# Kernel tuning notes

Hardware: AMD Instinct MI355X
Metric: run time of the kernel (lower is better)

## Reference

```python
import jax, jax.numpy as jnp
import numpy as np

B, T, I, H, E = 256, 128, 512, 1024, 256


def setup_inputs() -> dict:
    key = jax.random.key(0)
    ks = jax.random.split(key, 14)
    s = lambda *d: 1.0 / np.sqrt(d[-1])
    inp = {
        "x": jax.random.normal(ks[0], (B, T, I), jnp.float32),
        # encoder LSTMCell(I, H): weights [4H, *], gate order i,f,g,o (torch)
        "enc_Wih": jax.random.uniform(ks[1], (4 * H, I), jnp.float32, -s(H), s(H)),
        "enc_Whh": jax.random.uniform(ks[2], (4 * H, H), jnp.float32, -s(H), s(H)),
        "enc_bih": jax.random.uniform(ks[3], (4 * H,), jnp.float32, -s(H), s(H)),
        "enc_bhh": jax.random.uniform(ks[4], (4 * H,), jnp.float32, -s(H), s(H)),
        # enc_fc: H -> E
        "encfc_W": jax.random.uniform(ks[5], (E, H), jnp.float32, -s(H), s(H)),
        "encfc_b": jax.random.uniform(ks[6], (E,), jnp.float32, -s(H), s(H)),
        # dec_fc: E -> H
        "decfc_W": jax.random.uniform(ks[7], (H, E), jnp.float32, -s(E), s(E)),
        "decfc_b": jax.random.uniform(ks[8], (H,), jnp.float32, -s(E), s(E)),
        # decoder LSTMCell(H + I, I)
        "dec_Wih": jax.random.uniform(ks[9], (4 * I, H + I), jnp.float32, -s(I), s(I)),
        "dec_Whh": jax.random.uniform(ks[10], (4 * I, I), jnp.float32, -s(I), s(I)),
        "dec_bih": jax.random.uniform(ks[11], (4 * I,), jnp.float32, -s(I), s(I)),
        "dec_bhh": jax.random.uniform(ks[12], (4 * I,), jnp.float32, -s(I), s(I)),
    }
    return inp


def _gates(pre):
    i, f, g, o = jnp.split(pre, 4, axis=-1)
    return jax.nn.sigmoid(i), jax.nn.sigmoid(f), jnp.tanh(g), jax.nn.sigmoid(o)


def reference(x, enc_Wih, enc_Whh, enc_bih, enc_bhh, encfc_W, encfc_b,
              decfc_W, decfc_b, dec_Wih, dec_Whh, dec_bih, dec_bhh):
    b = x.shape[0]
    # ---- encoder: precompute input projections for all timesteps ----
    x_proj = jnp.einsum('btd,gd->tbg', x, enc_Wih) + (enc_bih + enc_bhh)  # [T,B,4H]

    def enc_step(carry, xp):
        h, c = carry
        i, f, g, o = _gates(xp + h @ enc_Whh.T)
        c = f * c + i * g
        h = o * jnp.tanh(c)
        return (h, c), None

    h0 = jnp.zeros((b, H), x.dtype)
    c0 = jnp.zeros((b, H), x.dtype)
    (_, c_final), _ = jax.lax.scan(enc_step, (h0, c0), x_proj)

    # NB: original code names the returned (h, c) as (o_t_enc, h_t_enc), so
    # embd is computed from the final CELL state -- replicated faithfully.
    embd = jax.nn.relu(c_final @ encfc_W.T + encfc_b)                # [B,E]
    dec_first_hidden = jax.nn.relu(embd @ decfc_W.T + decfc_b)       # [B,H]

    # ---- decoder: input at each step is cat(dec_first_hidden, h_prev) ----
    # (eval path: teacher forcing disabled; dec states init to zeros)
    fixed = dec_first_hidden @ dec_Wih[:, :H].T + (dec_bih + dec_bhh)  # [B,4I]
    W_rec = dec_Wih[:, H:] + dec_Whh  # input second-half and hidden are both h_prev

    def dec_step(carry, _):
        h, c = carry
        i, f, g, o = _gates(fixed + h @ W_rec.T)
        c = f * c + i * g
        h = o * jnp.tanh(c)
        return (h, c), h

    hd0 = jnp.zeros((b, I), x.dtype)
    cd0 = jnp.zeros((b, I), x.dtype)
    _, hs = jax.lax.scan(dec_step, (hd0, cd0), None, length=x.shape[1])  # [T,B,I]
    outputs = jnp.transpose(hs[::-1], (1, 0, 2))  # reversed, [B,T,I]
    return outputs, embd
```

## Files before the change

### kernel.cpp

```cpp
#include <hip/hip_runtime.h>
#include <hip/hip_fp16.h>


#define B_ 256
#define T_ 128
#define I_ 512
#define H_ 1024
#define E_ 256

#define ENC_STEP 262144
#define DEC_STEP 131072
#define SENT32 0x7C7C7C7Cu

typedef _Float16 half8 __attribute__((ext_vector_type(8)));
typedef float floatx4 __attribute__((ext_vector_type(4)));

__device__ __forceinline__ float sigmoidf_(float x) { return 1.0f / (1.0f + __expf(-x)); }
__device__ __forceinline__ float tanhf_(float x) {
    x = fminf(fmaxf(x, -15.0f), 15.0f);
    float e = __expf(2.0f * x);
    return (e - 1.0f) / (e + 1.0f);
}

union HU { unsigned long long u[2]; half8 h; };

__device__ __forceinline__ void ld_chunk(const _Float16* p, HU& v) {
    const unsigned long long* q = (const unsigned long long*)p;
    v.u[0] = __hip_atomic_load(q,     __ATOMIC_RELAXED, __HIP_MEMORY_SCOPE_AGENT);
    v.u[1] = __hip_atomic_load(q + 1, __ATOMIC_RELAXED, __HIP_MEMORY_SCOPE_AGENT);
}
__device__ __forceinline__ int chunk_ok(const HU& v) {
    unsigned a = (unsigned)v.u[0], b = (unsigned)(v.u[0] >> 32);
    unsigned c = (unsigned)v.u[1], d = (unsigned)(v.u[1] >> 32);
    return (int)((a != SENT32) & (b != SENT32) & (c != SENT32) & (d != SENT32));
}
template <int STRIDE>
__device__ __forceinline__ void load_grp(const _Float16* base, HU v[4]) {
#pragma unroll
    for (int m = 0; m < 4; ++m) ld_chunk(base + (size_t)m * STRIDE, v[m]);
}
template <int STRIDE>
__device__ __forceinline__ void fix_grp(const _Float16* base, HU v[4]) {
    while (!(chunk_ok(v[0]) & chunk_ok(v[1]) & chunk_ok(v[2]) & chunk_ok(v[3]))) {
        __builtin_amdgcn_s_sleep(1);
        load_grp<STRIDE>(base, v);
    }
}

__device__ __forceinline__ half8 ldg_h8_sc1(const _Float16* p) {
    HU v; ld_chunk(p, v); return v.h;
}
__device__ __forceinline__ void stg_h2_sc1(_Float16* p, float a, float b) {
    union { _Float16 h[2]; unsigned int u; } v;
    v.h[0] = (_Float16)a; v.h[1] = (_Float16)b;
    __hip_atomic_store((unsigned int*)p, v.u, __ATOMIC_RELAXED, __HIP_MEMORY_SCOPE_AGENT);
}
__device__ __forceinline__ void wait_vm0() {
    asm volatile("s_waitcnt vmcnt(0)" ::: "memory");
}
__device__ __forceinline__ void poll_rg(int* flags, int rgbase, int lane, int target) {
    while (__hip_atomic_load(&flags[rgbase + lane], __ATOMIC_RELAXED, __HIP_MEMORY_SCOPE_AGENT) < target)
        __builtin_amdgcn_s_sleep(1);
    asm volatile("" ::: "memory");
}

__global__ void shuffle_x_kernel(const float* __restrict__ x, _Float16* __restrict__ xf) {
    const int gg   = blockIdx.x * 256 + threadIdx.x;
    const int tile = gg >> 6;
    const int lane = gg & 63;
    const int t  = tile >> 8;
    const int rt = (tile >> 4) & 15;
    const int kc = tile & 15;
    const int b  = rt * 16 + (lane & 15);
    const int j0 = kc * 32 + ((lane >> 4) << 3);
    const float* src = x + ((size_t)b * T_ + t) * I_ + j0;
    float4 f0 = *(const float4*)src;
    float4 f1 = *(const float4*)(src + 4);
    half8 h = { (_Float16)f0.x, (_Float16)f0.y, (_Float16)f0.z, (_Float16)f0.w,
                (_Float16)f1.x, (_Float16)f1.y, (_Float16)f1.z, (_Float16)f1.w };
    *(half8*)(xf + (size_t)tile * 512 + lane * 8) = h;
}

__global__ __launch_bounds__(256) void small_gemm_kernel(
    const float* __restrict__ A, int lda,
    const float* __restrict__ W, int ldw,
    const float* __restrict__ b1, const float* __restrict__ b2,
    float* __restrict__ out, int N, int K, int relu)
{
    __shared__ float sA2[32][33];
    __shared__ float sW2[32][33];
    int tid = threadIdx.x;
    int tx = tid & 15, ty = tid >> 4;
    int m0 = blockIdx.y * 32, n0 = blockIdx.x * 32;
    float acc[2][2] = {};
    for (int k0 = 0; k0 < K; k0 += 32) {
        __syncthreads();
#pragma unroll
        for (int i = 0; i < 4; ++i) {
            int e = tid + i * 256;
            int r = e >> 5, c = e & 31;
            sA2[r][c] = A[(size_t)(m0 + r) * lda + k0 + c];
            sW2[r][c] = W[(size_t)(n0 + r) * ldw + k0 + c];
        }
        __syncthreads();
#pragma unroll
        for (int k = 0; k < 32; ++k) {
            float a0 = sA2[ty * 2][k], a1 = sA2[ty * 2 + 1][k];
            float w0 = sW2[tx * 2][k], w1 = sW2[tx * 2 + 1][k];
            acc[0][0] += a0 * w0; acc[0][1] += a0 * w1;
            acc[1][0] += a1 * w0; acc[1][1] += a1 * w1;
        }
    }
#pragma unroll
    for (int i = 0; i < 2; ++i)
#pragma unroll
        for (int j = 0; j < 2; ++j) {
            int m = m0 + ty * 2 + i, n = n0 + tx * 2 + j;
            float v = acc[i][j] + b1[n] + (b2 ? b2[n] : 0.0f);
            if (relu) v = fmaxf(v, 0.0f);
            out[(size_t)m * N + n] = v;
        }
}

__global__ __launch_bounds__(256, 1) void enc_persist(
    const _Float16* __restrict__ xf,
    const float* __restrict__ Wih, const float* __restrict__ Whh,
    const float* __restrict__ bih, const float* __restrict__ bhh,
    _Float16* __restrict__ hbuf, float* __restrict__ c_out, int* __restrict__ flags)
{
    const int tid  = threadIdx.x;
    const int wave = tid >> 6, lane = tid & 63;
    const int q = lane >> 4, n15 = lane & 15;
    const int blk = blockIdx.x;
    const int rg = blk >> 6, cc = blk & 63;

    half8 bw[4][12];
#pragma unroll
    for (int g = 0; g < 4; ++g) {
        const int jc = g * H_ + cc * 16 + n15;
#pragma unroll
        for (int kc = 0; kc < 12; ++kc) {
            const int k = (4 * kc + wave) * 32 + q * 8;
            const float* src = (k < I_) ? (Wih + (size_t)jc * I_ + k)
                                        : (Whh + (size_t)jc * H_ + (k - I_));
            float4 f0 = *(const float4*)src;
            float4 f1 = *(const float4*)(src + 4);
            bw[g][kc] = half8{(_Float16)f0.x, (_Float16)f0.y, (_Float16)f0.z, (_Float16)f0.w,
                              (_Float16)f1.x, (_Float16)f1.y, (_Float16)f1.z, (_Float16)f1.w};
        }
    }

    const int hcp = tid & 7;
    const int rT  = tid >> 3;
    float breg[4][2];
#pragma unroll
    for (int g = 0; g < 4; ++g)
#pragma unroll
        for (int e = 0; e < 2; ++e) {
            const int j = g * H_ + cc * 16 + 2 * hcp + e;
            breg[g][e] = bih[j] + bhh[j];
        }
    float creg[2][2] = {{0.f, 0.f}, {0.f, 0.f}};

    __shared__ float preT[4][64][35];
    const size_t laneoff = (size_t)lane * 8;

    for (int s = 0; s < T_; ++s) {
        const _Float16* __restrict__ hcur = hbuf + (size_t)(s & 1) * 262144;
        _Float16* __restrict__ hnxt = hbuf + (size_t)((s + 1) & 1) * 262144;

        floatx4 acc[4][4];
#pragma unroll
        for (int m = 0; m < 4; ++m)
#pragma unroll
            for (int n = 0; n < 4; ++n) acc[m][n] = floatx4{0.f, 0.f, 0.f, 0.f};

        half8 X[4][4];
#pragma unroll
        for (int kc = 0; kc < 4; ++kc)
#pragma unroll
            for (int m = 0; m < 4; ++m)
                X[kc][m] = *(const half8*)(xf + (((size_t)s * 16 + rg * 4 + m) * 16
                                                + (4 * kc + wave)) * 512 + laneoff);
#pragma unroll
        for (int kc = 0; kc < 2; ++kc)
#pragma unroll
            for (int n = 0; n < 4; ++n)
#pragma unroll
                for (int m = 0; m < 4; ++m)
                    acc[m][n] = __builtin_amdgcn_mfma_f32_16x16x32_f16(
                        X[kc][m], bw[n][kc], acc[m][n], 0, 0, 0);

        poll_rg(flags, rg * 64, lane, 4 * s);

        half8 Hb[4][4];
#pragma unroll
        for (int kc = 4; kc < 8; ++kc)
#pragma unroll
            for (int m = 0; m < 4; ++m)
                Hb[kc - 4][m] = ldg_h8_sc1(hcur + ((size_t)(rg * 4 + m) * 32
                                                   + (4 * kc + wave - 16)) * 512 + laneoff);

#pragma unroll
        for (int kc = 2; kc < 4; ++kc)
#pragma unroll
            for (int n = 0; n < 4; ++n)
#pragma unroll
                for (int m = 0; m < 4; ++m)
                    acc[m][n] = __builtin_amdgcn_mfma_f32_16x16x32_f16(
                        X[kc][m], bw[n][kc], acc[m][n], 0, 0, 0);

#pragma unroll
        for (int kc = 4; kc < 12; ++kc) {
            const int sl = kc & 3;
#pragma unroll
            for (int n = 0; n < 4; ++n)
#pragma unroll
                for (int m = 0; m < 4; ++m)
                    acc[m][n] = __builtin_amdgcn_mfma_f32_16x16x32_f16(
                        Hb[sl][m], bw[n][kc], acc[m][n], 0, 0, 0);
            if (kc < 8) {
#pragma unroll
                for (int m = 0; m < 4; ++m)
                    Hb[sl][m] = ldg_h8_sc1(hcur + ((size_t)(rg * 4 + m) * 32
                                                   + (4 * (kc + 4) + wave - 16)) * 512 + laneoff);
            }
        }

#pragma unroll
        for (int p = 0; p < 2; ++p) {
            if (p) __syncthreads();
#pragma unroll
            for (int m = 0; m < 2; ++m)
#pragma unroll
                for (int n = 0; n < 4; ++n)
#pragma unroll
                    for (int r = 0; r < 4; ++r)
                        preT[wave][n * 16 + n15][m * 16 + q * 4 + r] = acc[p * 2 + m][n][r];
            __syncthreads();
            float pg[4][2];
#pragma unroll
            for (int g = 0; g < 4; ++g)
#pragma unroll
                for (int e = 0; e < 2; ++e) {
                    const int col = g * 16 + 2 * hcp + e;
                    pg[g][e] = preT[0][col][rT] + preT[1][col][rT]
                             + preT[2][col][rT] + preT[3][col][rT] + breg[g][e];
                }
            float hv[2];
#pragma unroll
            for (int e = 0; e < 2; ++e) {
                const float ig = sigmoidf_(pg[0][e]);
                const float fg = sigmoidf_(pg[1][e]);
                const float gg = tanhf_(pg[2][e]);
                const float og = sigmoidf_(pg[3][e]);
                const float c  = fg * creg[p][e] + ig * gg;
                creg[p][e] = c;
                hv[e] = og * tanhf_(c);
            }
            const int row = p * 32 + rT;
            const int j   = cc * 16 + 2 * hcp;
            const int kch = j >> 5, j5 = j & 31;
            const int lt  = (row & 15) | ((j5 >> 3) << 4);
            stg_h2_sc1(hnxt + ((size_t)(rg * 4 + (row >> 4)) * 32 + kch) * 512
                            + lt * 8 + (j5 & 7), hv[0], hv[1]);
        }

        wait_vm0();
        if (lane == 0)
            __hip_atomic_fetch_add(&flags[blk], 1, __ATOMIC_RELAXED, __HIP_MEMORY_SCOPE_AGENT);
        __syncthreads();
    }

#pragma unroll
    for (int p = 0; p < 2; ++p)
        *(float2*)(c_out + (size_t)(rg * 64 + p * 32 + rT) * H_ + cc * 16 + 2 * hcp)
            = float2{creg[p][0], creg[p][1]};
}

__global__ __launch_bounds__(256, 1) void dec_df(
    const float* __restrict__ dWih, const float* __restrict__ dWhh,
    const float* __restrict__ fixedb,
    _Float16* __restrict__ hbuf, float* __restrict__ out)
{
    const int tid  = threadIdx.x;
    const int wave = tid >> 6, lane = tid & 63;
    const int q = lane >> 4, n15 = lane & 15;
    const int blk = blockIdx.x;
    const int rg = blk >> 6, cc = blk & 63;

    half8 bw[2][4];
#pragma unroll
    for (int n = 0; n < 2; ++n) {
        const int jc = (n * 2 + (n15 >> 3)) * I_ + cc * 8 + (n15 & 7);
#pragma unroll
        for (int kc = 0; kc < 4; ++kc) {
            const int k = wave * 128 + kc * 32 + q * 8;
            const float* s0 = dWih + (size_t)jc * (H_ + I_) + H_ + k;
            const float* s1 = dWhh + (size_t)jc * I_ + k;
            float4 a0 = *(const float4*)s0, a1 = *(const float4*)(s0 + 4);
            float4 b0 = *(const float4*)s1, b1 = *(const float4*)(s1 + 4);
            bw[n][kc] = half8{(_Float16)(a0.x + b0.x), (_Float16)(a0.y + b0.y),
                              (_Float16)(a0.z + b0.z), (_Float16)(a0.w + b0.w),
                              (_Float16)(a1.x + b1.x), (_Float16)(a1.y + b1.y),
                              (_Float16)(a1.z + b1.z), (_Float16)(a1.w + b1.w)};
        }
    }

    const int hcp = tid & 3;
    const int rT  = tid >> 2;
    const int brow = rg * 64 + rT;
    float fx[4][2];
#pragma unroll
    for (int g = 0; g < 4; ++g)
#pragma unroll
        for (int e = 0; e < 2; ++e)
            fx[g][e] = fixedb[(size_t)brow * (4 * I_) + g * I_ + cc * 8 + 2 * hcp + e];
    float creg2[2] = {0.f, 0.f};

    __shared__ float preT[4][32][67];
    const size_t laneoff = (size_t)lane * 8;

    for (int s = 0; s < T_; ++s) {
        const _Float16* __restrict__ hcur = hbuf + (size_t)s * DEC_STEP;
        _Float16* __restrict__ hnxt = hbuf + (size_t)(s + 1) * DEC_STEP;

        HU Hb[4][4];
#pragma unroll
        for (int kc = 0; kc < 4; ++kc)
            load_grp<16 * 512>(hcur + ((size_t)(rg * 4) * 16 + (wave * 4 + kc)) * 512
                                    + laneoff, Hb[kc]);

        floatx4 acc[4][2];
#pragma unroll
        for (int m = 0; m < 4; ++m)
#pragma unroll
            for (int n = 0; n < 2; ++n) acc[m][n] = floatx4{0.f, 0.f, 0.f, 0.f};
#pragma unroll
        for (int kc = 0; kc < 4; ++kc) {
            fix_grp<16 * 512>(hcur + ((size_t)(rg * 4) * 16 + (wave * 4 + kc)) * 512
                                   + laneoff, Hb[kc]);
#pragma unroll
            for (int n = 0; n < 2; ++n)
#pragma unroll
                for (int m = 0; m < 4; ++m)
                    acc[m][n] = __builtin_amdgcn_mfma_f32_16x16x32_f16(
                        Hb[kc][m].h, bw[n][kc], acc[m][n], 0, 0, 0);
        }

#pragma unroll
        for (int p = 0; p < 2; ++p) {
            if (p) __syncthreads();
#pragma unroll
            for (int m = 0; m < 2; ++m)
#pragma unroll
                for (int n = 0; n < 2; ++n)
#pragma unroll
                    for (int r = 0; r < 4; ++r)
                        preT[wave][n * 16 + n15][m * 16 + q * 4 + r] = acc[p * 2 + m][n][r];
            __syncthreads();
            if ((rT >> 5) == p) {
                const int rl = rT & 31;
                float pg[4][2];
#pragma unroll
                for (int g = 0; g < 4; ++g)
#pragma unroll
                    for (int e = 0; e < 2; ++e) {
                        const int col = (g >> 1) * 16 + (g & 1) * 8 + 2 * hcp + e;
                        pg[g][e] = preT[0][col][rl] + preT[1][col][rl]
                                 + preT[2][col][rl] + preT[3][col][rl] + fx[g][e];
                    }
                float hv[2];
#pragma unroll
                for (int e = 0; e < 2; ++e) {
                    const float ig = sigmoidf_(pg[0][e]);
                    const float fg = sigmoidf_(pg[1][e]);
                    const float gg = tanhf_(pg[2][e]);
                    const float og = sigmoidf_(pg[3][e]);
                    const float c  = fg * creg2[e] + ig * gg;
                    creg2[e] = c;
                    hv[e] = og * tanhf_(c);
                }
                *(float2*)(out + ((size_t)brow * T_ + (T_ - 1 - s)) * I_ + cc * 8 + 2 * hcp)
                    = float2{hv[0], hv[1]};
                const int j = cc * 8 + 2 * hcp;
                const int kch = j >> 5, j5 = j & 31;
                const int lt  = (rT & 15) | ((j5 >> 3) << 4);
                stg_h2_sc1(hnxt + ((size_t)(rg * 4 + (rT >> 4)) * 16 + kch) * 512
                                + lt * 8 + (j5 & 7), hv[0], hv[1]);
            }
        }
        __syncthreads();
    }
}

__global__ __launch_bounds__(256, 1) void dec_persist(
    const float* __restrict__ dWih, const float* __restrict__ dWhh,
    const float* __restrict__ fixedb,
    _Float16* __restrict__ hbuf, float* __restrict__ out, int* __restrict__ flags)
{
    const int tid  = threadIdx.x;
    const int wave = tid >> 6, lane = tid & 63;
    const int q = lane >> 4, n15 = lane & 15;
    const int blk = blockIdx.x;
    const int rg = blk >> 6, cc = blk & 63;

    half8 bw[2][4];
#pragma unroll
    for (int n = 0; n < 2; ++n) {
        const int jc = (n * 2 + (n15 >> 3)) * I_ + cc * 8 + (n15 & 7);
#pragma unroll
        for (int kc = 0; kc < 4; ++kc) {
            const int k = wave * 128 + kc * 32 + q * 8;
            const float* s0 = dWih + (size_t)jc * (H_ + I_) + H_ + k;
            const float* s1 = dWhh + (size_t)jc * I_ + k;
            float4 a0 = *(const float4*)s0, a1 = *(const float4*)(s0 + 4);
            float4 b0 = *(const float4*)s1, b1 = *(const float4*)(s1 + 4);
            bw[n][kc] = half8{(_Float16)(a0.x + b0.x), (_Float16)(a0.y + b0.y),
                              (_Float16)(a0.z + b0.z), (_Float16)(a0.w + b0.w),
                              (_Float16)(a1.x + b1.x), (_Float16)(a1.y + b1.y),
                              (_Float16)(a1.z + b1.z), (_Float16)(a1.w + b1.w)};
        }
    }

    const int hcp = tid & 3;
    const int rT  = tid >> 2;
    const int brow = rg * 64 + rT;
    float fx[4][2];
#pragma unroll
    for (int g = 0; g < 4; ++g)
#pragma unroll
        for (int e = 0; e < 2; ++e)
            fx[g][e] = fixedb[(size_t)brow * (4 * I_) + g * I_ + cc * 8 + 2 * hcp + e];
    float creg2[2] = {0.f, 0.f};

    __shared__ float preT[4][32][67];
    const size_t laneoff = (size_t)lane * 8;

    for (int s = 0; s < T_; ++s) {
        const _Float16* __restrict__ hcur = hbuf + (size_t)(s & 1) * 131072;
        _Float16* __restrict__ hnxt = hbuf + (size_t)((s + 1) & 1) * 131072;

        poll_rg(flags, rg * 64, lane, s);

        half8 Hb[4][4];
#pragma unroll
        for (int kc = 0; kc < 4; ++kc)
#pragma unroll
            for (int m = 0; m < 4; ++m)
                Hb[kc][m] = ldg_h8_sc1(hcur + ((size_t)(rg * 4 + m) * 16
                                               + (wave * 4 + kc)) * 512 + laneoff);
        floatx4 acc[4][2];
#pragma unroll
        for (int m = 0; m < 4; ++m)
#pragma unroll
            for (int n = 0; n < 2; ++n) acc[m][n] = floatx4{0.f, 0.f, 0.f, 0.f};
#pragma unroll
        for (int kc = 0; kc < 4; ++kc)
#pragma unroll
            for (int n = 0; n < 2; ++n)
#pragma unroll
                for (int m = 0; m < 4; ++m)
                    acc[m][n] = __builtin_amdgcn_mfma_f32_16x16x32_f16(
                        Hb[kc][m], bw[n][kc], acc[m][n], 0, 0, 0);

#pragma unroll
        for (int p = 0; p < 2; ++p) {
            if (p) __syncthreads();
#pragma unroll
            for (int m = 0; m < 2; ++m)
#pragma unroll
                for (int n = 0; n < 2; ++n)
#pragma unroll
                    for (int r = 0; r < 4; ++r)
                        preT[wave][n * 16 + n15][m * 16 + q * 4 + r] = acc[p * 2 + m][n][r];
            __syncthreads();
            if ((rT >> 5) == p) {
                const int rl = rT & 31;
                float pg[4][2];
#pragma unroll
                for (int g = 0; g < 4; ++g)
#pragma unroll
                    for (int e = 0; e < 2; ++e) {
                        const int col = (g >> 1) * 16 + (g & 1) * 8 + 2 * hcp + e;
                        pg[g][e] = preT[0][col][rl] + preT[1][col][rl]
                                 + preT[2][col][rl] + preT[3][col][rl] + fx[g][e];
                    }
                float hv[2];
#pragma unroll
                for (int e = 0; e < 2; ++e) {
                    const float ig = sigmoidf_(pg[0][e]);
                    const float fg = sigmoidf_(pg[1][e]);
                    const float gg = tanhf_(pg[2][e]);
                    const float og = sigmoidf_(pg[3][e]);
                    const float c  = fg * creg2[e] + ig * gg;
                    creg2[e] = c;
                    hv[e] = og * tanhf_(c);
                }
                *(float2*)(out + ((size_t)brow * T_ + (T_ - 1 - s)) * I_ + cc * 8 + 2 * hcp)
                    = float2{hv[0], hv[1]};
                const int j = cc * 8 + 2 * hcp;
                const int kch = j >> 5, j5 = j & 31;
                const int lt  = (rT & 15) | ((j5 >> 3) << 4);
                stg_h2_sc1(hnxt + ((size_t)(rg * 4 + (rT >> 4)) * 16 + kch) * 512
                                + lt * 8 + (j5 & 7), hv[0], hv[1]);
            }
        }

        wait_vm0();
        __syncthreads();
        if (tid == 0)
            __hip_atomic_store(&flags[blk], s + 1, __ATOMIC_RELAXED, __HIP_MEMORY_SCOPE_AGENT);
    }
}

extern "C" void kernel_launch(void* const* d_in, const int* in_sizes, int n_in,
                              void* d_out_v, int out_size, void* d_ws, size_t ws_size,
                              hipStream_t stream) {
    (void)in_sizes; (void)n_in; (void)out_size;
    const float* x    = (const float*)d_in[0];
    const float* eWih = (const float*)d_in[1];
    const float* eWhh = (const float*)d_in[2];
    const float* ebih = (const float*)d_in[3];
    const float* ebhh = (const float*)d_in[4];
    const float* efcW = (const float*)d_in[5];
    const float* efcb = (const float*)d_in[6];
    const float* dfcW = (const float*)d_in[7];
    const float* dfcb = (const float*)d_in[8];
    const float* dWih = (const float*)d_in[9];
    const float* dWhh = (const float*)d_in[10];
    const float* dbih = (const float*)d_in[11];
    const float* dbhh = (const float*)d_in[12];
    float* d_out = (float*)d_out_v;

    char* ws = (char*)d_ws;
    size_t off = 0;
    auto carve = [&](size_t bytes) {
        char* p = ws + off;
        off += (bytes + 255) & ~(size_t)255;
        return p;
    };

    const size_t xf_b  = (size_t)B_ * T_ * I_ * 2;
    const size_t hbE_b = (size_t)2 * ENC_STEP * 2;
    const size_t hbD_b = (size_t)(T_ + 1) * DEC_STEP * 2;
    const size_t ce_b  = (size_t)B_ * H_ * 4;
    const size_t fxb_b = (size_t)B_ * 4 * I_ * 4;
    const size_t d1_b  = (size_t)B_ * H_ * 4;
    const size_t need_primary = xf_b + hbE_b + hbD_b + ce_b + fxb_b + d1_b + 8192;

    float* embd = d_out + (size_t)B_ * T_ * I_;

    if (ws_size == 0 || ws_size >= need_primary) {
        _Float16* xf     = (_Float16*)carve(xf_b);
        _Float16* hbufE  = (_Float16*)carve(hbE_b);
        _Float16* hbufD  = (_Float16*)carve(hbD_b);
        float*    c_e    = (float*)carve(ce_b);
        float*    fixedb = (float*)carve(fxb_b);
        float*    dec1   = (float*)carve(d1_b);
        int*      flagsE = (int*)carve(256 * 4);

        hipMemsetAsync(flagsE, 0, 256 * 4, stream);
        hipMemsetAsync(hbufE, 0, (size_t)ENC_STEP * 2, stream);
        hipMemsetAsync(hbufD, 0, (size_t)DEC_STEP * 2, stream);
        hipMemsetAsync((char*)hbufD + (size_t)DEC_STEP * 2, 0x7C, (size_t)T_ * DEC_STEP * 2, stream);

        shuffle_x_kernel<<<dim3(8192), 256, 0, stream>>>(x, xf);
        enc_persist<<<dim3(256), 256, 0, stream>>>(xf, eWih, eWhh, ebih, ebhh,
                                                   hbufE, c_e, flagsE);
        small_gemm_kernel<<<dim3(E_ / 32, B_ / 32), 256, 0, stream>>>(
            c_e, H_, efcW, H_, efcb, nullptr, embd, E_, H_, 1);
        small_gemm_kernel<<<dim3(H_ / 32, B_ / 32), 256, 0, stream>>>(
            embd, E_, dfcW, E_, dfcb, nullptr, dec1, H_, E_, 1);
        small_gemm_kernel<<<dim3(4 * I_ / 32, B_ / 32), 256, 0, stream>>>(
            dec1, H_, dWih, H_ + I_, dbih, dbhh, fixedb, 4 * I_, H_, 0);
        dec_df<<<dim3(256), 256, 0, stream>>>(dWih, dWhh, fixedb, hbufD, d_out);
    } else {
        _Float16* xf     = (_Float16*)carve(xf_b);
        _Float16* hbufE  = (_Float16*)carve((size_t)2 * ENC_STEP * 2);
        _Float16* hbufD  = (_Float16*)carve((size_t)2 * DEC_STEP * 2);
        float*    c_e    = (float*)carve(ce_b);
        float*    fixedb = (float*)carve(fxb_b);
        float*    dec1   = (float*)carve(d1_b);
        int*      flagsE = (int*)carve(256 * 4);
        int*      flagsD = (int*)carve(256 * 4);

        hipMemsetAsync(flagsE, 0, 256 * 4, stream);
        hipMemsetAsync(flagsD, 0, 256 * 4, stream);
        hipMemsetAsync(hbufE, 0, (size_t)ENC_STEP * 2, stream);
        hipMemsetAsync(hbufD, 0, (size_t)DEC_STEP * 2, stream);

        shuffle_x_kernel<<<dim3(8192), 256, 0, stream>>>(x, xf);
        enc_persist<<<dim3(256), 256, 0, stream>>>(xf, eWih, eWhh, ebih, ebhh,
                                                   hbufE, c_e, flagsE);
        small_gemm_kernel<<<dim3(E_ / 32, B_ / 32), 256, 0, stream>>>(
            c_e, H_, efcW, H_, efcb, nullptr, embd, E_, H_, 1);
        small_gemm_kernel<<<dim3(H_ / 32, B_ / 32), 256, 0, stream>>>(
            embd, E_, dfcW, E_, dfcb, nullptr, dec1, H_, E_, 1);
        small_gemm_kernel<<<dim3(4 * I_ / 32, B_ / 32), 256, 0, stream>>>(
            dec1, H_, dWih, H_ + I_, dbih, dbhh, fixedb, 4 * I_, H_, 0);
        dec_persist<<<dim3(256), 256, 0, stream>>>(dWih, dWhh, fixedb,
                                                   hbufD, d_out, flagsD);
    }
}
```

Before: 1.653 ms.

## Re-tile persistent encoder to 512-thread blocks with 32 rows by 32 hidden columns

The encoder persistent kernel now runs 8 waves per block, and each block owns a 32-row by 32-hidden-column tile instead of 64 rows by 16 columns. Each wave holds fewer K-slices of the weights and does less serial MFMA work per step. The new h values are staged in shared memory so they go out as coalesced 32-bit stores, and each block now waits on only 32 producer flags. The cost is a larger cross-wave reduction over 8 partial sums in LDS, and the fallback path keeps the old kernel under a new name.

```diff
diff --git a/kernel.cpp b/kernel.cpp
--- a/kernel.cpp
+++ b/kernel.cpp
@@ -22,7 +22,7 @@
     return (e - 1.0f) / (e + 1.0f);
 }
 
-union HU { unsigned long long u[2]; half8 h; };
+union HU { unsigned long long u[2]; unsigned v[4]; half8 h; };
 
 __device__ __forceinline__ void ld_chunk(const _Float16* p, HU& v) {
     const unsigned long long* q = (const unsigned long long*)p;
@@ -30,9 +30,8 @@
     v.u[1] = __hip_atomic_load(q + 1, __ATOMIC_RELAXED, __HIP_MEMORY_SCOPE_AGENT);
 }
 __device__ __forceinline__ int chunk_ok(const HU& v) {
-    unsigned a = (unsigned)v.u[0], b = (unsigned)(v.u[0] >> 32);
-    unsigned c = (unsigned)v.u[1], d = (unsigned)(v.u[1] >> 32);
-    return (int)((a != SENT32) & (b != SENT32) & (c != SENT32) & (d != SENT32));
+    return (int)((v.v[0] != SENT32) & (v.v[1] != SENT32)
+               & (v.v[2] != SENT32) & (v.v[3] != SENT32));
 }
 template <int STRIDE>
 __device__ __forceinline__ void load_grp(const _Float16* base, HU v[4]) {
@@ -54,6 +53,9 @@
     union { _Float16 h[2]; unsigned int u; } v;
     v.h[0] = (_Float16)a; v.h[1] = (_Float16)b;
     __hip_atomic_store((unsigned int*)p, v.u, __ATOMIC_RELAXED, __HIP_MEMORY_SCOPE_AGENT);
+}
+__device__ __forceinline__ void stg_u32_sc1(_Float16* p, unsigned v) {
+    __hip_atomic_store((unsigned int*)p, v, __ATOMIC_RELAXED, __HIP_MEMORY_SCOPE_AGENT);
 }
 __device__ __forceinline__ void wait_vm0() {
     asm volatile("s_waitcnt vmcnt(0)" ::: "memory");
@@ -122,7 +124,7 @@
         }
 }
 
-__global__ __launch_bounds__(256, 1) void enc_persist(
+__global__ __launch_bounds__(512, 1) void enc_w512(
     const _Float16* __restrict__ xf,
     const float* __restrict__ Wih, const float* __restrict__ Whh,
     const float* __restrict__ bih, const float* __restrict__ bhh,
@@ -132,138 +134,127 @@
     const int wave = tid >> 6, lane = tid & 63;
     const int q = lane >> 4, n15 = lane & 15;
     const int blk = blockIdx.x;
-    const int rg = blk >> 6, cc = blk & 63;
-
-    half8 bw[4][12];
-#pragma unroll
-    for (int g = 0; g < 4; ++g) {
-        const int jc = g * H_ + cc * 16 + n15;
-#pragma unroll
-        for (int kc = 0; kc < 12; ++kc) {
-            const int k = (4 * kc + wave) * 32 + q * 8;
+    const int rg  = blk >> 5;
+    const int cc2 = blk & 31;
+
+    half8 bw[8][6];
+#pragma unroll
+    for (int n = 0; n < 8; ++n) {
+        const int jc = (n >> 1) * H_ + cc2 * 32 + (n & 1) * 16 + n15;
+#pragma unroll
+        for (int kk = 0; kk < 6; ++kk) {
+            const int k = (8 * kk + wave) * 32 + q * 8;
             const float* src = (k < I_) ? (Wih + (size_t)jc * I_ + k)
                                         : (Whh + (size_t)jc * H_ + (k - I_));
             float4 f0 = *(const float4*)src;
             float4 f1 = *(const float4*)(src + 4);
-            bw[g][kc] = half8{(_Float16)f0.x, (_Float16)f0.y, (_Float16)f0.z, (_Float16)f0.w,
+            bw[n][kk] = half8{(_Float16)f0.x, (_Float16)f0.y, (_Float16)f0.z, (_Float16)f0.w,
                               (_Float16)f1.x, (_Float16)f1.y, (_Float16)f1.z, (_Float16)f1.w};
         }
     }
 
-    const int hcp = tid & 7;
-    const int rT  = tid >> 3;
-    float breg[4][2];
-#pragma unroll
-    for (int g = 0; g < 4; ++g)
-#pragma unroll
-        for (int e = 0; e < 2; ++e) {
-            const int j = g * H_ + cc * 16 + 2 * hcp + e;
-            breg[g][e] = bih[j] + bhh[j];
-        }
-    float creg[2][2] = {{0.f, 0.f}, {0.f, 0.f}};
-
-    __shared__ float preT[4][64][35];
+    const int hcol_l = tid >> 4;
+    const int rowl   = tid & 15;
+    float breg[4];
+#pragma unroll
+    for (int g = 0; g < 4; ++g) {
+        const int j = g * H_ + cc2 * 32 + hcol_l;
+        breg[g] = bih[j] + bhh[j];
+    }
+    float creg[2] = {0.f, 0.f};
+
+    __shared__ float preT[8][128][20];
+    __shared__ unsigned short hsh[32][32];
     const size_t laneoff = (size_t)lane * 8;
 
     for (int s = 0; s < T_; ++s) {
-        const _Float16* __restrict__ hcur = hbuf + (size_t)(s & 1) * 262144;
-        _Float16* __restrict__ hnxt = hbuf + (size_t)((s + 1) & 1) * 262144;
-
-        floatx4 acc[4][4];
-#pragma unroll
-        for (int m = 0; m < 4; ++m)
-#pragma unroll
-            for (int n = 0; n < 4; ++n) acc[m][n] = floatx4{0.f, 0.f, 0.f, 0.f};
-
-        half8 X[4][4];
-#pragma unroll
-        for (int kc = 0; kc < 4; ++kc)
-#pragma unroll
-            for (int m = 0; m < 4; ++m)
-                X[kc][m] = *(const half8*)(xf + (((size_t)s * 16 + rg * 4 + m) * 16
-                                                + (4 * kc + wave)) * 512 + laneoff);
-#pragma unroll
-        for (int kc = 0; kc < 2; ++kc)
-#pragma unroll
-            for (int n = 0; n < 4; ++n)
-#pragma unroll
-                for (int m = 0; m < 4; ++m)
+        const _Float16* __restrict__ hcur = hbuf + (size_t)(s & 1) * ENC_STEP;
+        _Float16* __restrict__ hnxt = hbuf + (size_t)((s + 1) & 1) * ENC_STEP;
+
+        floatx4 acc[2][8];
+#pragma unroll
+        for (int m = 0; m < 2; ++m)
+#pragma unroll
+            for (int n = 0; n < 8; ++n) acc[m][n] = floatx4{0.f, 0.f, 0.f, 0.f};
+
+        half8 X[2][2];
+#pragma unroll
+        for (int kk = 0; kk < 2; ++kk)
+#pragma unroll
+            for (int m = 0; m < 2; ++m)
+                X[kk][m] = *(const half8*)(xf + (((size_t)s * 16 + rg * 2 + m) * 16
+                                                + (8 * kk + wave)) * 512 + laneoff);
+#pragma unroll
+        for (int n = 0; n < 8; ++n)
+#pragma unroll
+            for (int m = 0; m < 2; ++m)
+                acc[m][n] = __builtin_amdgcn_mfma_f32_16x16x32_f16(
+                    X[0][m], bw[n][0], acc[m][n], 0, 0, 0);
+
+        poll_rg(flags, rg * 32, lane & 31, 8 * s);
+
+        half8 Hb[4][2];
+#pragma unroll
+        for (int k = 0; k < 4; ++k)
+#pragma unroll
+            for (int m = 0; m < 2; ++m)
+                Hb[k][m] = ldg_h8_sc1(hcur + ((size_t)(rg * 2 + m) * 32
+                                              + (8 * k + wave)) * 512 + laneoff);
+
+#pragma unroll
+        for (int n = 0; n < 8; ++n)
+#pragma unroll
+            for (int m = 0; m < 2; ++m)
+                acc[m][n] = __builtin_amdgcn_mfma_f32_16x16x32_f16(
+                    X[1][m], bw[n][1], acc[m][n], 0, 0, 0);
+
+#pragma unroll
+        for (int kk = 2; kk < 6; ++kk)
+#pragma unroll
+            for (int n = 0; n < 8; ++n)
+#pragma unroll
+                for (int m = 0; m < 2; ++m)
                     acc[m][n] = __builtin_amdgcn_mfma_f32_16x16x32_f16(
-                        X[kc][m], bw[n][kc], acc[m][n], 0, 0, 0);
-
-        poll_rg(flags, rg * 64, lane, 4 * s);
-
-        half8 Hb[4][4];
-#pragma unroll
-        for (int kc = 4; kc < 8; ++kc)
-#pragma unroll
-            for (int m = 0; m < 4; ++m)
-                Hb[kc - 4][m] = ldg_h8_sc1(hcur + ((size_t)(rg * 4 + m) * 32
-                                                   + (4 * kc + wave - 16)) * 512 + laneoff);
-
-#pragma unroll
-        for (int kc = 2; kc < 4; ++kc)
-#pragma unroll
-            for (int n = 0; n < 4; ++n)
-#pragma unroll
-                for (int m = 0; m < 4; ++m)
-                    acc[m][n] = __builtin_amdgcn_mfma_f32_16x16x32_f16(
-                        X[kc][m], bw[n][kc], acc[m][n], 0, 0, 0);
-
-#pragma unroll
-        for (int kc = 4; kc < 12; ++kc) {
-            const int sl = kc & 3;
-#pragma unroll
-            for (int n = 0; n < 4; ++n)
-#pragma unroll
-                for (int m = 0; m < 4; ++m)
-                    acc[m][n] = __builtin_amdgcn_mfma_f32_16x16x32_f16(
-                        Hb[sl][m], bw[n][kc], acc[m][n], 0, 0, 0);
-            if (kc < 8) {
-#pragma unroll
-                for (int m = 0; m < 4; ++m)
-                    Hb[sl][m] = ldg_h8_sc1(hcur + ((size_t)(rg * 4 + m) * 32
-                                                   + (4 * (kc + 4) + wave - 16)) * 512 + laneoff);
-            }
-        }
+                        Hb[kk - 2][m], bw[n][kk], acc[m][n], 0, 0, 0);
 
 #pragma unroll
         for (int p = 0; p < 2; ++p) {
             if (p) __syncthreads();
 #pragma unroll
-            for (int m = 0; m < 2; ++m)
-#pragma unroll
-                for (int n = 0; n < 4; ++n)
-#pragma unroll
-                    for (int r = 0; r < 4; ++r)
-                        preT[wave][n * 16 + n15][m * 16 + q * 4 + r] = acc[p * 2 + m][n][r];
+            for (int n = 0; n < 8; ++n) {
+                const int cpre = (n >> 1) * 32 + (n & 1) * 16 + n15;
+                *(floatx4*)&preT[wave][cpre][q * 4] = acc[p][n];
+            }
             __syncthreads();
-            float pg[4][2];
-#pragma unroll
-            for (int g = 0; g < 4; ++g)
-#pragma unroll
-                for (int e = 0; e < 2; ++e) {
-                    const int col = g * 16 + 2 * hcp + e;
-                    pg[g][e] = preT[0][col][rT] + preT[1][col][rT]
-                             + preT[2][col][rT] + preT[3][col][rT] + breg[g][e];
-                }
-            float hv[2];
-#pragma unroll
-            for (int e = 0; e < 2; ++e) {
-                const float ig = sigmoidf_(pg[0][e]);
-                const float fg = sigmoidf_(pg[1][e]);
-                const float gg = tanhf_(pg[2][e]);
-                const float og = sigmoidf_(pg[3][e]);
-                const float c  = fg * creg[p][e] + ig * gg;
-                creg[p][e] = c;
-                hv[e] = og * tanhf_(c);
+            float pg[4];
+#pragma unroll
+            for (int g = 0; g < 4; ++g) {
+                float v = breg[g];
+#pragma unroll
+                for (int w = 0; w < 8; ++w)
+                    v += preT[w][g * 32 + hcol_l][rowl];
+                pg[g] = v;
             }
-            const int row = p * 32 + rT;
-            const int j   = cc * 16 + 2 * hcp;
-            const int kch = j >> 5, j5 = j & 31;
-            const int lt  = (row & 15) | ((j5 >> 3) << 4);
-            stg_h2_sc1(hnxt + ((size_t)(rg * 4 + (row >> 4)) * 32 + kch) * 512
-                            + lt * 8 + (j5 & 7), hv[0], hv[1]);
+            const float ig = sigmoidf_(pg[0]);
+            const float fg = sigmoidf_(pg[1]);
+            const float gg = tanhf_(pg[2]);
+            const float og = sigmoidf_(pg[3]);
+            const float c  = fg * creg[p] + ig * gg;
+            creg[p] = c;
+            const float hv = og * tanhf_(c);
+            union { _Float16 f; unsigned short u; } cv;
+            cv.f = (_Float16)hv;
+            hsh[p * 16 + rowl][hcol_l] = cv.u;
+        }
+        __syncthreads();
+
+        {
+            const int row = tid >> 4;
+            const int jp  = tid & 15;
+            const unsigned v = *(const unsigned*)&hsh[row][2 * jp];
+            const int lt = (row & 15) | ((jp >> 2) << 4);
+            stg_u32_sc1(hnxt + ((size_t)(rg * 2 + (row >> 4)) * 32 + cc2) * 512
+                             + lt * 8 + ((2 * jp) & 7), v);
         }
 
         wait_vm0();
@@ -274,8 +265,7 @@
 
 #pragma unroll
     for (int p = 0; p < 2; ++p)
-        *(float2*)(c_out + (size_t)(rg * 64 + p * 32 + rT) * H_ + cc * 16 + 2 * hcp)
-            = float2{creg[p][0], creg[p][1]};
+        c_out[(size_t)(rg * 32 + p * 16 + rowl) * H_ + cc2 * 32 + hcol_l] = creg[p];
 }
 
 __global__ __launch_bounds__(256, 1) void dec_df(
@@ -394,6 +384,152 @@
     }
 }
 
+__global__ __launch_bounds__(256, 1) void enc_ring(
+    const _Float16* __restrict__ xf,
+    const float* __restrict__ Wih, const float* __restrict__ Whh,
+    const float* __restrict__ bih, const float* __restrict__ bhh,
+    _Float16* __restrict__ hbuf, float* __restrict__ c_out, int* __restrict__ flags)
+{
+    const int tid  = threadIdx.x;
+    const int wave = tid >> 6, lane = tid & 63;
+    const int q = lane >> 4, n15 = lane & 15;
+    const int blk = blockIdx.x;
+    const int rg = blk >> 6, cc = blk & 63;
+
+    half8 bw[4][12];
+#pragma unroll
+    for (int g = 0; g < 4; ++g) {
+        const int jc = g * H_ + cc * 16 + n15;
+#pragma unroll
+        for (int kc = 0; kc < 12; ++kc) {
+            const int k = (4 * kc + wave) * 32 + q * 8;
+            const float* src = (k < I_) ? (Wih + (size_t)jc * I_ + k)
+                                        : (Whh + (size_t)jc * H_ + (k - I_));
+            float4 f0 = *(const float4*)src;
+            float4 f1 = *(const float4*)(src + 4);
+            bw[g][kc] = half8{(_Float16)f0.x, (_Float16)f0.y, (_Float16)f0.z, (_Float16)f0.w,
+                              (_Float16)f1.x, (_Float16)f1.y, (_Float16)f1.z, (_Float16)f1.w};
+        }
+    }
+
+    const int hcp = tid & 7;
+    const int rT  = tid >> 3;
+    float breg[4][2];
+#pragma unroll
+    for (int g = 0; g < 4; ++g)
+#pragma unroll
+        for (int e = 0; e < 2; ++e) {
+            const int j = g * H_ + cc * 16 + 2 * hcp + e;
+            breg[g][e] = bih[j] + bhh[j];
+        }
+    float creg[2][2] = {{0.f, 0.f}, {0.f, 0.f}};
+
+    __shared__ float preT[4][64][35];
+    const size_t laneoff = (size_t)lane * 8;
+
+    for (int s = 0; s < T_; ++s) {
+        const _Float16* __restrict__ hcur = hbuf + (size_t)(s & 1) * ENC_STEP;
+        _Float16* __restrict__ hnxt = hbuf + (size_t)((s + 1) & 1) * ENC_STEP;
+
+        floatx4 acc[4][4];
+#pragma unroll
+        for (int m = 0; m < 4; ++m)
+#pragma unroll
+            for (int n = 0; n < 4; ++n) acc[m][n] = floatx4{0.f, 0.f, 0.f, 0.f};
+
+        half8 X[4][4];
+#pragma unroll
+        for (int kc = 0; kc < 4; ++kc)
+#pragma unroll
+            for (int m = 0; m < 4; ++m)
+                X[kc][m] = *(const half8*)(xf + (((size_t)s * 16 + rg * 4 + m) * 16
+                                                + (4 * kc + wave)) * 512 + laneoff);
+#pragma unroll
+        for (int kc = 0; kc < 4; ++kc)
+#pragma unroll
+            for (int n = 0; n < 4; ++n)
+#pragma unroll
+                for (int m = 0; m < 4; ++m)
+                    acc[m][n] = __builtin_amdgcn_mfma_f32_16x16x32_f16(
+                        X[kc][m], bw[n][kc], acc[m][n], 0, 0, 0);
+
+        poll_rg(flags, rg * 64, lane, 4 * s);
+
+        half8 Hb[4][4];
+#pragma unroll
+        for (int kc = 4; kc < 8; ++kc)
+#pragma unroll
+            for (int m = 0; m < 4; ++m)
+                Hb[kc - 4][m] = ldg_h8_sc1(hcur + ((size_t)(rg * 4 + m) * 32
+                                                   + (4 * kc + wave - 16)) * 512 + laneoff);
+#pragma unroll
+        for (int kc = 4; kc < 12; ++kc) {
+            const int sl = kc & 3;
+#pragma unroll
+            for (int n = 0; n < 4; ++n)
+#pragma unroll
+                for (int m = 0; m < 4; ++m)
+                    acc[m][n] = __builtin_amdgcn_mfma_f32_16x16x32_f16(
+                        Hb[sl][m], bw[n][kc], acc[m][n], 0, 0, 0);
+            if (kc < 8) {
+#pragma unroll
+                for (int m = 0; m < 4; ++m)
+                    Hb[sl][m] = ldg_h8_sc1(hcur + ((size_t)(rg * 4 + m) * 32
+                                                   + (4 * (kc + 4) + wave - 16)) * 512 + laneoff);
+            }
+        }
+
+#pragma unroll
+        for (int p = 0; p < 2; ++p) {
+            if (p) __syncthreads();
+#pragma unroll
+            for (int m = 0; m < 2; ++m)
+#pragma unroll
+                for (int n = 0; n < 4; ++n)
+#pragma unroll
+                    for (int r = 0; r < 4; ++r)
+                        preT[wave][n * 16 + n15][m * 16 + q * 4 + r] = acc[p * 2 + m][n][r];
+            __syncthreads();
+            float pg[4][2];
+#pragma unroll
+            for (int g = 0; g < 4; ++g)
+#pragma unroll
+                for (int e = 0; e < 2; ++e) {
+                    const int col = g * 16 + 2 * hcp + e;
+                    pg[g][e] = preT[0][col][rT] + preT[1][col][rT]
+                             + preT[2][col][rT] + preT[3][col][rT] + breg[g][e];
+                }
+            float hv[2];
+#pragma unroll
+            for (int e = 0; e < 2; ++e) {
+                const float ig = sigmoidf_(pg[0][e]);
+                const float fg = sigmoidf_(pg[1][e]);
+                const float gg = tanhf_(pg[2][e]);
+                const float og = sigmoidf_(pg[3][e]);
+                const float c  = fg * creg[p][e] + ig * gg;
+                creg[p][e] = c;
+                hv[e] = og * tanhf_(c);
+            }
+            const int row = p * 32 + rT;
+            const int j   = cc * 16 + 2 * hcp;
+            const int kch = j >> 5, j5 = j & 31;
+            const int lt  = (row & 15) | ((j5 >> 3) << 4);
+            stg_h2_sc1(hnxt + ((size_t)(rg * 4 + (row >> 4)) * 32 + kch) * 512
+                            + lt * 8 + (j5 & 7), hv[0], hv[1]);
+        }
+
+        wait_vm0();
+        if (lane == 0)
+            __hip_atomic_fetch_add(&flags[blk], 1, __ATOMIC_RELAXED, __HIP_MEMORY_SCOPE_AGENT);
+        __syncthreads();
+    }
+
+#pragma unroll
+    for (int p = 0; p < 2; ++p)
+        *(float2*)(c_out + (size_t)(rg * 64 + p * 32 + rT) * H_ + cc * 16 + 2 * hcp)
+            = float2{creg[p][0], creg[p][1]};
+}
+
 __global__ __launch_bounds__(256, 1) void dec_persist(
     const float* __restrict__ dWih, const float* __restrict__ dWhh,
     const float* __restrict__ fixedb,
@@ -438,8 +574,8 @@
     const size_t laneoff = (size_t)lane * 8;
 
     for (int s = 0; s < T_; ++s) {
-        const _Float16* __restrict__ hcur = hbuf + (size_t)(s & 1) * 131072;
-        _Float16* __restrict__ hnxt = hbuf + (size_t)((s + 1) & 1) * 131072;
+        const _Float16* __restrict__ hcur = hbuf + (size_t)(s & 1) * DEC_STEP;
+        _Float16* __restrict__ hnxt = hbuf + (size_t)((s + 1) & 1) * DEC_STEP;
 
         poll_rg(flags, rg * 64, lane, s);
 
@@ -566,8 +702,8 @@
         hipMemsetAsync((char*)hbufD + (size_t)DEC_STEP * 2, 0x7C, (size_t)T_ * DEC_STEP * 2, stream);
 
         shuffle_x_kernel<<<dim3(8192), 256, 0, stream>>>(x, xf);
-        enc_persist<<<dim3(256), 256, 0, stream>>>(xf, eWih, eWhh, ebih, ebhh,
-                                                   hbufE, c_e, flagsE);
+        enc_w512<<<dim3(256), 512, 0, stream>>>(xf, eWih, eWhh, ebih, ebhh,
+                                                hbufE, c_e, flagsE);
         small_gemm_kernel<<<dim3(E_ / 32, B_ / 32), 256, 0, stream>>>(
             c_e, H_, efcW, H_, efcb, nullptr, embd, E_, H_, 1);
         small_gemm_kernel<<<dim3(H_ / 32, B_ / 32), 256, 0, stream>>>(
@@ -591,8 +727,8 @@
         hipMemsetAsync(hbufD, 0, (size_t)DEC_STEP * 2, stream);
 
         shuffle_x_kernel<<<dim3(8192), 256, 0, stream>>>(x, xf);
-        enc_persist<<<dim3(256), 256, 0, stream>>>(xf, eWih, eWhh, ebih, ebhh,
-                                                   hbufE, c_e, flagsE);
+        enc_ring<<<dim3(256), 256, 0, stream>>>(xf, eWih, eWhh, ebih, ebhh,
+                                                hbufE, c_e, flagsE);
         small_gemm_kernel<<<dim3(E_ / 32, B_ / 32), 256, 0, stream>>>(
             c_e, H_, efcW, H_, efcb, nullptr, embd, E_, H_, 1);
         small_gemm_kernel<<<dim3(H_ / 32, B_ / 32), 256, 0, stream>>>(
```

Measured after the change: 3.408 ms. 106% more time.

## Halve decoder persistent grid by giving each block 16 hidden columns

Applied to the files above, without the earlier changes.

The dataflow decoder kernel now runs on 128 blocks instead of 256, with each block computing 16 hidden columns across all four gates (a 4x4 MFMA accumulator tile) rather than 8. All 256 threads now take part in the gate epilogue for both row halves, and the per-thread bias and cell state grow to match. The aim is to cut the number of consumers polling the sentinel-filled h buffer each step and to reuse each loaded h fragment across twice as many MFMAs. The cost is more serial MFMA and epilogue work per block on each recurrent step, with half the CUs left idle.

```diff
diff --git a/kernel.cpp b/kernel.cpp
--- a/kernel.cpp
+++ b/kernel.cpp
@@ -22,7 +22,7 @@
     return (e - 1.0f) / (e + 1.0f);
 }
 
-union HU { unsigned long long u[2]; half8 h; };
+union HU { unsigned long long u[2]; unsigned v[4]; half8 h; };
 
 __device__ __forceinline__ void ld_chunk(const _Float16* p, HU& v) {
     const unsigned long long* q = (const unsigned long long*)p;
@@ -30,9 +30,8 @@
     v.u[1] = __hip_atomic_load(q + 1, __ATOMIC_RELAXED, __HIP_MEMORY_SCOPE_AGENT);
 }
 __device__ __forceinline__ int chunk_ok(const HU& v) {
-    unsigned a = (unsigned)v.u[0], b = (unsigned)(v.u[0] >> 32);
-    unsigned c = (unsigned)v.u[1], d = (unsigned)(v.u[1] >> 32);
-    return (int)((a != SENT32) & (b != SENT32) & (c != SENT32) & (d != SENT32));
+    return (int)((v.v[0] != SENT32) & (v.v[1] != SENT32)
+               & (v.v[2] != SENT32) & (v.v[3] != SENT32));
 }
 template <int STRIDE>
 __device__ __forceinline__ void load_grp(const _Float16* base, HU v[4]) {
@@ -166,8 +165,8 @@
     const size_t laneoff = (size_t)lane * 8;
 
     for (int s = 0; s < T_; ++s) {
-        const _Float16* __restrict__ hcur = hbuf + (size_t)(s & 1) * 262144;
-        _Float16* __restrict__ hnxt = hbuf + (size_t)((s + 1) & 1) * 262144;
+        const _Float16* __restrict__ hcur = hbuf + (size_t)(s & 1) * ENC_STEP;
+        _Float16* __restrict__ hnxt = hbuf + (size_t)((s + 1) & 1) * ENC_STEP;
 
         floatx4 acc[4][4];
 #pragma unroll
@@ -278,7 +277,7 @@
             = float2{creg[p][0], creg[p][1]};
 }
 
-__global__ __launch_bounds__(256, 1) void dec_df(
+__global__ __launch_bounds__(256, 1) void dec_df2(
     const float* __restrict__ dWih, const float* __restrict__ dWhh,
     const float* __restrict__ fixedb,
     _Float16* __restrict__ hbuf, float* __restrict__ out)
@@ -287,12 +286,13 @@
     const int wave = tid >> 6, lane = tid & 63;
     const int q = lane >> 4, n15 = lane & 15;
     const int blk = blockIdx.x;
-    const int rg = blk >> 6, cc = blk & 63;
-
-    half8 bw[2][4];
-#pragma unroll
-    for (int n = 0; n < 2; ++n) {
-        const int jc = (n * 2 + (n15 >> 3)) * I_ + cc * 8 + (n15 & 7);
+    const int rg = blk >> 5;
+    const int cc = blk & 31;
+
+    half8 bw[4][4];
+#pragma unroll
+    for (int n = 0; n < 4; ++n) {
+        const int jc = n * I_ + cc * 16 + n15;
 #pragma unroll
         for (int kc = 0; kc < 4; ++kc) {
             const int k = wave * 128 + kc * 32 + q * 8;
@@ -307,18 +307,20 @@
         }
     }
 
-    const int hcp = tid & 3;
-    const int rT  = tid >> 2;
-    const int brow = rg * 64 + rT;
-    float fx[4][2];
-#pragma unroll
-    for (int g = 0; g < 4; ++g)
-#pragma unroll
-        for (int e = 0; e < 2; ++e)
-            fx[g][e] = fixedb[(size_t)brow * (4 * I_) + g * I_ + cc * 8 + 2 * hcp + e];
-    float creg2[2] = {0.f, 0.f};
-
-    __shared__ float preT[4][32][67];
+    const int hcp = tid & 7;
+    const int rT  = tid >> 3;
+    float fx[2][4][2];
+#pragma unroll
+    for (int p = 0; p < 2; ++p)
+#pragma unroll
+        for (int g = 0; g < 4; ++g)
+#pragma unroll
+            for (int e = 0; e < 2; ++e)
+                fx[p][g][e] = fixedb[(size_t)(rg * 64 + p * 32 + rT) * (4 * I_)
+                                     + g * I_ + cc * 16 + 2 * hcp + e];
+    float creg2[2][2] = {{0.f, 0.f}, {0.f, 0.f}};
+
+    __shared__ float preT[4][64][35];
     const size_t laneoff = (size_t)lane * 8;
 
     for (int s = 0; s < T_; ++s) {
@@ -331,17 +333,17 @@
             load_grp<16 * 512>(hcur + ((size_t)(rg * 4) * 16 + (wave * 4 + kc)) * 512
                                     + laneoff, Hb[kc]);
 
-        floatx4 acc[4][2];
+        floatx4 acc[4][4];
 #pragma unroll
         for (int m = 0; m < 4; ++m)
 #pragma unroll
-            for (int n = 0; n < 2; ++n) acc[m][n] = floatx4{0.f, 0.f, 0.f, 0.f};
+            for (int n = 0; n < 4; ++n) acc[m][n] = floatx4{0.f, 0.f, 0.f, 0.f};
 #pragma unroll
         for (int kc = 0; kc < 4; ++kc) {
             fix_grp<16 * 512>(hcur + ((size_t)(rg * 4) * 16 + (wave * 4 + kc)) * 512
                                    + laneoff, Hb[kc]);
 #pragma unroll
-            for (int n = 0; n < 2; ++n)
+            for (int n = 0; n < 4; ++n)
 #pragma unroll
                 for (int m = 0; m < 4; ++m)
                     acc[m][n] = __builtin_amdgcn_mfma_f32_16x16x32_f16(
@@ -354,41 +356,39 @@
 #pragma unroll
             for (int m = 0; m < 2; ++m)
 #pragma unroll
-                for (int n = 0; n < 2; ++n)
+                for (int n = 0; n < 4; ++n)
 #pragma unroll
                     for (int r = 0; r < 4; ++r)
                         preT[wave][n * 16 + n15][m * 16 + q * 4 + r] = acc[p * 2 + m][n][r];
             __syncthreads();
-            if ((rT >> 5) == p) {
-                const int rl = rT & 31;
-                float pg[4][2];
-#pragma unroll
-                for (int g = 0; g < 4; ++g)
-#pragma unroll
-                    for (int e = 0; e < 2; ++e) {
-                        const int col = (g >> 1) * 16 + (g & 1) * 8 + 2 * hcp + e;
-                        pg[g][e] = preT[0][col][rl] + preT[1][col][rl]
-                                 + preT[2][col][rl] + preT[3][col][rl] + fx[g][e];
-                    }
-                float hv[2];
+            float pg[4][2];
+#pragma unroll
+            for (int g = 0; g < 4; ++g)
 #pragma unroll
                 for (int e = 0; e < 2; ++e) {
-                    const float ig = sigmoidf_(pg[0][e]);
-                    const float fg = sigmoidf_(pg[1][e]);
-                    const float gg = tanhf_(pg[2][e]);
-                    const float og = sigmoidf_(pg[3][e]);
-                    const float c  = fg * creg2[e] + ig * gg;
-                    creg2[e] = c;
-                    hv[e] = og * tanhf_(c);
+                    const int col = g * 16 + 2 * hcp + e;
+                    pg[g][e] = preT[0][col][rT] + preT[1][col][rT]
+                             + preT[2][col][rT] + preT[3][col][rT] + fx[p][g][e];
                 }
-                *(float2*)(out + ((size_t)brow * T_ + (T_ - 1 - s)) * I_ + cc * 8 + 2 * hcp)
-                    = float2{hv[0], hv[1]};
-                const int j = cc * 8 + 2 * hcp;
-                const int kch = j >> 5, j5 = j & 31;
-                const int lt  = (rT & 15) | ((j5 >> 3) << 4);
-                stg_h2_sc1(hnxt + ((size_t)(rg * 4 + (rT >> 4)) * 16 + kch) * 512
-                                + lt * 8 + (j5 & 7), hv[0], hv[1]);
+            float hv[2];
+#pragma unroll
+            for (int e = 0; e < 2; ++e) {
+                const float ig = sigmoidf_(pg[0][e]);
+                const float fg = sigmoidf_(pg[1][e]);
+                const float gg = tanhf_(pg[2][e]);
+                const float og = sigmoidf_(pg[3][e]);
+                const float c  = fg * creg2[p][e] + ig * gg;
+                creg2[p][e] = c;
+                hv[e] = og * tanhf_(c);
             }
+            const int row = p * 32 + rT;
+            *(float2*)(out + ((size_t)(rg * 64 + row) * T_ + (T_ - 1 - s)) * I_
+                           + cc * 16 + 2 * hcp) = float2{hv[0], hv[1]};
+            const int j   = cc * 16 + 2 * hcp;
+            const int kch = j >> 5, j5 = j & 31;
+            const int lt  = (row & 15) | ((j5 >> 3) << 4);
+            stg_h2_sc1(hnxt + ((size_t)(rg * 4 + (row >> 4)) * 16 + kch) * 512
+                            + lt * 8 + (j5 & 7), hv[0], hv[1]);
         }
         __syncthreads();
     }
@@ -438,8 +438,8 @@
     const size_t laneoff = (size_t)lane * 8;
 
     for (int s = 0; s < T_; ++s) {
-        const _Float16* __restrict__ hcur = hbuf + (size_t)(s & 1) * 131072;
-        _Float16* __restrict__ hnxt = hbuf + (size_t)((s + 1) & 1) * 131072;
+        const _Float16* __restrict__ hcur = hbuf + (size_t)(s & 1) * DEC_STEP;
+        _Float16* __restrict__ hnxt = hbuf + (size_t)((s + 1) & 1) * DEC_STEP;
 
         poll_rg(flags, rg * 64, lane, s);
 
@@ -574,7 +574,7 @@
             embd, E_, dfcW, E_, dfcb, nullptr, dec1, H_, E_, 1);
         small_gemm_kernel<<<dim3(4 * I_ / 32, B_ / 32), 256, 0, stream>>>(
             dec1, H_, dWih, H_ + I_, dbih, dbhh, fixedb, 4 * I_, H_, 0);
-        dec_df<<<dim3(256), 256, 0, stream>>>(dWih, dWhh, fixedb, hbufD, d_out);
+        dec_df2<<<dim3(128), 256, 0, stream>>>(dWih, dWhh, fixedb, hbufD, d_out);
     } else {
         _Float16* xf     = (_Float16*)carve(xf_b);
         _Float16* hbufE  = (_Float16*)carve((size_t)2 * ENC_STEP * 2);
```

New measurement: 1.688 ms. 1.02x slower.
